# Performance work log

Hardware: AMD Instinct MI355X
Metric: run time of the kernel (lower is better)

Reference implementation:

```python
import jax, jax.numpy as jnp
import numpy as np

B, N, F, UNITS = 8, 2048, 64, 64

def setup_inputs() -> dict:
    key = jax.random.key(0)
    ks = jax.random.split(key, 7)
    inputs = jax.random.normal(ks[0], (B, N, F), dtype=jnp.float32)
    Dynamic_L = jax.random.normal(ks[1], (B, N, N), dtype=jnp.float32)
    W = jax.random.uniform(ks[2], (B, N, N, 3), dtype=jnp.float32)
    Geo = jax.random.normal(ks[3], (N, N), dtype=jnp.float32)
    KL = jax.random.normal(ks[4], (N, N), dtype=jnp.float32)
    # Dense(Units, tanh) params (glorot-ish scale)
    Wd = jax.random.normal(ks[5], (F, UNITS), dtype=jnp.float32) / np.sqrt(F)
    bd = jnp.zeros((UNITS,), dtype=jnp.float32)
    return {"inputs": inputs, "Dynamic_L": Dynamic_L, "W": W,
            "Geo": Geo, "KL": KL, "Wd": Wd, "bd": bd}

def reference(inputs, Dynamic_L, W, Geo, KL, Wd, bd):
    # Weighted fusion of three N x N matrices; Geo/KL broadcast over batch.
    Fusion = Dynamic_L * W[..., 0] + Geo[None] * W[..., 1] + KL[None] * W[..., 2]  # [B,N,N]
    Fusion = jax.nn.softmax(Fusion, axis=-1)
    G1 = jnp.einsum('bnm,bmf->bnf', Fusion, inputs)  # graph matmul [B,N,F]
    return jnp.tanh(G1 @ Wd + bd)  # Dense(Units, tanh) -> [B,N,UNITS]
```

## Files before the change

kernel.cpp:

```cpp
#include <hip/hip_runtime.h>
#include <hip/hip_fp16.h>

#define Nn 2048
#define Ff 64
#define Uu 64
#define NT 256
#define CW 256
#define NCH 8

typedef _Float16 f16x4 __attribute__((ext_vector_type(4)));
typedef _Float16 f16x8 __attribute__((ext_vector_type(8)));
typedef float    f32x4 __attribute__((ext_vector_type(4)));

#define MFMA32(a,b,c) __builtin_amdgcn_mfma_f32_16x16x32_f16(a,b,c,0,0,0)
#define G1S 68

__global__ __launch_bounds__(256) void transposeX(const float* __restrict__ X,
                                                  _Float16* __restrict__ Xt) {
    __shared__ _Float16 tile[64][65];
    const int b = blockIdx.x, kt = blockIdx.y;
    #pragma unroll
    for (int i = 0; i < 16; ++i) {
        int e  = i * 256 + threadIdx.x;
        int kk = e >> 6, ff = e & 63;
        tile[ff][kk] = (_Float16)X[((size_t)b * Nn + kt * 64 + kk) * Ff + ff];
    }
    __syncthreads();
    #pragma unroll
    for (int i = 0; i < 16; ++i) {
        int e  = i * 256 + threadIdx.x;
        int ff = e >> 6, kk = e & 63;
        Xt[((size_t)b * Ff + ff) * Nn + kt * 64 + kk] = tile[ff][kk];
    }
}

#define ISSUE_U(Vd,Vw0,Vw1,Vw2,Vg,Vk, C, U) {                 \
    const size_t _o = (size_t)(U) * Nn + (size_t)(C) * CW + (lane << 2); \
    Vd  = *(const float4*)(dP + _o);                          \
    Vw0 = *(const float4*)(wP + 3 * _o);                      \
    Vw1 = *(const float4*)(wP + 3 * _o + 4);                  \
    Vw2 = *(const float4*)(wP + 3 * _o + 8);                  \
    Vg  = *(const float4*)(gP + _o);                          \
    Vk  = *(const float4*)(kP + _o);                          \
}

#define CONSUME_U(Vd,Vw0,Vw1,Vw2,Vg,Vk, BUF, U) {                             \
    float _e0 = __expf(fminf(Vd.x*Vw0.x + Vg.x*Vw0.y + Vk.x*Vw0.z, 11.f));    \
    float _e1 = __expf(fminf(Vd.y*Vw0.w + Vg.y*Vw1.x + Vk.y*Vw1.y, 11.f));    \
    float _e2 = __expf(fminf(Vd.z*Vw1.z + Vg.z*Vw1.w + Vk.z*Vw2.x, 11.f));    \
    float _e3 = __expf(fminf(Vd.w*Vw2.y + Vg.w*Vw2.z + Vk.w*Vw2.w, 11.f));    \
    f16x4 _h = {(_Float16)_e0, (_Float16)_e1, (_Float16)_e2, (_Float16)_e3};  \
    rs[U] += (float)_h[0] + (float)_h[1] + (float)_h[2] + (float)_h[3];       \
    const int _ba = (p8 + (U)) * 512 + (lane << 3);                           \
    *(f16x4*)((char*)(BUF) + (_ba ^ (((U) & 7) << 4))) = _h;                  \
}

#define STAGE_BODY(BUF, C, PRE) {                          \
    CONSUME_U(Ad,Aw0,Aw1,Aw2,Ag,Ak, BUF, 0);               \
    ISSUE_U(Ad,Aw0,Aw1,Aw2,Ag,Ak, C, 2);                   \
    CONSUME_U(Bd,Bw0,Bw1,Bw2,Bg,Bk, BUF, 1);               \
    ISSUE_U(Bd,Bw0,Bw1,Bw2,Bg,Bk, C, 3);                   \
    CONSUME_U(Ad,Aw0,Aw1,Aw2,Ag,Ak, BUF, 2);               \
    ISSUE_U(Ad,Aw0,Aw1,Aw2,Ag,Ak, C, 4);                   \
    CONSUME_U(Bd,Bw0,Bw1,Bw2,Bg,Bk, BUF, 3);               \
    ISSUE_U(Bd,Bw0,Bw1,Bw2,Bg,Bk, C, 5);                   \
    CONSUME_U(Ad,Aw0,Aw1,Aw2,Ag,Ak, BUF, 4);               \
    ISSUE_U(Ad,Aw0,Aw1,Aw2,Ag,Ak, C, 6);                   \
    CONSUME_U(Bd,Bw0,Bw1,Bw2,Bg,Bk, BUF, 5);               \
    ISSUE_U(Bd,Bw0,Bw1,Bw2,Bg,Bk, C, 7);                   \
    CONSUME_U(Ad,Aw0,Aw1,Aw2,Ag,Ak, BUF, 6);               \
    if (PRE) { ISSUE_U(Ad,Aw0,Aw1,Aw2,Ag,Ak, (C)+1, 0); }  \
    CONSUME_U(Bd,Bw0,Bw1,Bw2,Bg,Bk, BUF, 7);               \
    if (PRE) { ISSUE_U(Bd,Bw0,Bw1,Bw2,Bg,Bk, (C)+1, 1); }  \
}

#define MFMA_CHUNK(BUF, C) {                                        \
    const char* _bc = (const char*)(BUF);                           \
    const _Float16* _x0 = xB0 + (size_t)(C) * CW;                   \
    const _Float16* _x1 = xB1 + (size_t)(C) * CW;                   \
    _Pragma("unroll")                                               \
    for (int kk = 0; kk < 8; ++kk) {                                \
        const int aa = r * 512 + kk * 64 + kg * 16;                 \
        f16x8 af = *(const f16x8*)(_bc + (aa ^ ((r & 7) << 4)));    \
        f16x8 b0 = *(const f16x8*)(_x0 + kk * 32);                  \
        f16x8 b1 = *(const f16x8*)(_x1 + kk * 32);                  \
        acc0 = MFMA32(af, b0, acc0);                                \
        acc1 = MFMA32(af, b1, acc1);                                \
    }                                                               \
}

__global__ __launch_bounds__(NT, 4) void fused_gcn(
    const _Float16* __restrict__ Xt,
    const float* __restrict__ Dyn,
    const float* __restrict__ Wf,
    const float* __restrict__ Geo,
    const float* __restrict__ KLm,
    const float* __restrict__ Wd,
    const float* __restrict__ bdv,
    float* __restrict__ out)
{
    __shared__ _Float16 Pb[2][16 * CW];
    __shared__ float wsumS[16];
    __shared__ float invS[16];
    __shared__ float g1[16 * G1S];

    const int t    = threadIdx.x;
    const int lane = t & 63;
    const int wid  = t >> 6;
    const int r    = lane & 15;
    const int kg   = lane >> 4;
    const int b    = blockIdx.x >> 7;
    const int n0   = (blockIdx.x & 127) << 4;

    const int p  = wid & 1;
    const int p8 = p << 3;
    const float* dP = Dyn + ((size_t)b * Nn + n0 + p8) * Nn;
    const float* wP = Wf  + ((size_t)b * Nn + n0 + p8) * (size_t)Nn * 3;
    const float* gP = Geo + (size_t)(n0 + p8) * Nn;
    const float* kP = KLm + (size_t)(n0 + p8) * Nn;

    const int cw = wid & 1;
    const _Float16* xB0 = Xt + (size_t)b * Ff * Nn
                        + (size_t)((cw * 2) * 16 + r) * Nn + (kg << 3);
    const _Float16* xB1 = xB0 + (size_t)16 * Nn;

    float rs[8] = {0.f,0.f,0.f,0.f,0.f,0.f,0.f,0.f};
    f32x4 acc0 = {0.f,0.f,0.f,0.f}, acc1 = {0.f,0.f,0.f,0.f};
    float4 Ad, Aw0, Aw1, Aw2, Ag, Ak;
    float4 Bd, Bw0, Bw1, Bw2, Bg, Bk;

    if (wid < 2) {
        ISSUE_U(Ad,Aw0,Aw1,Aw2,Ag,Ak, 0, 0);
        ISSUE_U(Bd,Bw0,Bw1,Bw2,Bg,Bk, 0, 1);
    }

    #pragma unroll 1
    for (int it = 0; it < NCH + 1; ++it) {
        if (wid < 2) {
            if (it < NCH) STAGE_BODY(&Pb[it & 1][0], it, (it + 1 < NCH));
        } else {
            if (it > 0) MFMA_CHUNK(&Pb[(it - 1) & 1][0], it - 1);
        }
        __syncthreads();
    }

    if (wid < 2) {
        #pragma unroll
        for (int u = 0; u < 8; ++u) {
            float v = rs[u];
            v += __shfl_xor(v, 1, 64);  v += __shfl_xor(v, 2, 64);
            v += __shfl_xor(v, 4, 64);  v += __shfl_xor(v, 8, 64);
            v += __shfl_xor(v, 16, 64); v += __shfl_xor(v, 32, 64);
            if (lane == 0) wsumS[p8 + u] = v;
        }
    }
    __syncthreads();
    if (t < 16) invS[t] = 1.0f / wsumS[t];
    __syncthreads();

    if (wid >= 2) {
        #pragma unroll
        for (int i = 0; i < 4; ++i) {
            const int ro = (kg << 2) + i;
            const float inv = invS[ro];
            g1[ro * G1S + (cw * 2) * 16 + r]       = acc0[i] * inv;
            g1[ro * G1S + (cw * 2 + 1) * 16 + r]   = acc1[i] * inv;
        }
    }
    __syncthreads();

    const int row0 = wid << 2;
    const float* g1r = g1 + row0 * G1S;
    float o0 = bdv[lane], o1 = o0, o2 = o0, o3 = o0;
    #pragma unroll 4
    for (int f = 0; f < Ff; ++f) {
        float wdv = Wd[f * Uu + lane];
        o0 += g1r[f]           * wdv;
        o1 += g1r[G1S + f]     * wdv;
        o2 += g1r[2 * G1S + f] * wdv;
        o3 += g1r[3 * G1S + f] * wdv;
    }
    float oo[4] = {o0, o1, o2, o3};
    #pragma unroll
    for (int i = 0; i < 4; ++i) {
        float x  = fminf(fmaxf(oo[i], -15.f), 15.f);
        float ex = __expf(2.f * x);
        out[((size_t)b * Nn + n0 + row0 + i) * Uu + lane] = (ex - 1.f) / (ex + 1.f);
    }
}

extern "C" void kernel_launch(void* const* d_in, const int* in_sizes, int n_in,
                              void* d_out, int out_size, void* d_ws, size_t ws_size,
                              hipStream_t stream) {
    const float* X   = (const float*)d_in[0];
    const float* Dyn = (const float*)d_in[1];
    const float* Wf  = (const float*)d_in[2];
    const float* Geo = (const float*)d_in[3];
    const float* KLm = (const float*)d_in[4];
    const float* Wd  = (const float*)d_in[5];
    const float* bdv = (const float*)d_in[6];
    float* out = (float*)d_out;

    _Float16* Xt = (_Float16*)d_ws;
    transposeX<<<dim3(8, Nn / 64), dim3(256), 0, stream>>>(X, Xt);
    fused_gcn<<<dim3(8 * (Nn / 16)), dim3(NT), 0, stream>>>(
        Xt, Dyn, Wf, Geo, KLm, Wd, bdv, out);
}
```

Measured before the change: 158.7 us.

## Stage inputs via global_load_lds double buffering with all waves computing

Replaces the producer/consumer wave split, where two waves computed exponentials and two ran MFMAs, with all four waves doing both. The Dyn/W/Geo/KL tiles are staged through direct global-to-LDS loads into double buffers. The chunk width shrinks to 64 columns over 32 iterations, and launch bounds drop to 2 blocks per SM to fit the larger LDS footprint. The aim is to hide HBM latency with asynchronous LDS loads and put all waves to work, at the cost of two barriers per much smaller chunk, more LDS use and possibly lower occupancy.

```diff
diff --git a/kernel.cpp b/kernel.cpp
--- a/kernel.cpp
+++ b/kernel.cpp
@@ -5,15 +5,19 @@
 #define Ff 64
 #define Uu 64
 #define NT 256
-#define CW 256
-#define NCH 8
+#define CW 64
+#define NCH 32
+#define G1S 68
 
 typedef _Float16 f16x4 __attribute__((ext_vector_type(4)));
 typedef _Float16 f16x8 __attribute__((ext_vector_type(8)));
 typedef float    f32x4 __attribute__((ext_vector_type(4)));
 
 #define MFMA32(a,b,c) __builtin_amdgcn_mfma_f32_16x16x32_f16(a,b,c,0,0,0)
-#define G1S 68
+
+#define GLD16(gp, lp) __builtin_amdgcn_global_load_lds(                      \
+    (const __attribute__((address_space(1))) void*)(gp),                     \
+    (__attribute__((address_space(3))) void*)(lp), 16, 0, 0)
 
 __global__ __launch_bounds__(256) void transposeX(const float* __restrict__ X,
                                                   _Float16* __restrict__ Xt) {
@@ -34,62 +38,22 @@
     }
 }
 
-#define ISSUE_U(Vd,Vw0,Vw1,Vw2,Vg,Vk, C, U) {                 \
-    const size_t _o = (size_t)(U) * Nn + (size_t)(C) * CW + (lane << 2); \
-    Vd  = *(const float4*)(dP + _o);                          \
-    Vw0 = *(const float4*)(wP + 3 * _o);                      \
-    Vw1 = *(const float4*)(wP + 3 * _o + 4);                  \
-    Vw2 = *(const float4*)(wP + 3 * _o + 8);                  \
-    Vg  = *(const float4*)(gP + _o);                          \
-    Vk  = *(const float4*)(kP + _o);                          \
-}
-
-#define CONSUME_U(Vd,Vw0,Vw1,Vw2,Vg,Vk, BUF, U) {                             \
-    float _e0 = __expf(fminf(Vd.x*Vw0.x + Vg.x*Vw0.y + Vk.x*Vw0.z, 11.f));    \
-    float _e1 = __expf(fminf(Vd.y*Vw0.w + Vg.y*Vw1.x + Vk.y*Vw1.y, 11.f));    \
-    float _e2 = __expf(fminf(Vd.z*Vw1.z + Vg.z*Vw1.w + Vk.z*Vw2.x, 11.f));    \
-    float _e3 = __expf(fminf(Vd.w*Vw2.y + Vg.w*Vw2.z + Vk.w*Vw2.w, 11.f));    \
-    f16x4 _h = {(_Float16)_e0, (_Float16)_e1, (_Float16)_e2, (_Float16)_e3};  \
-    rs[U] += (float)_h[0] + (float)_h[1] + (float)_h[2] + (float)_h[3];       \
-    const int _ba = (p8 + (U)) * 512 + (lane << 3);                           \
-    *(f16x4*)((char*)(BUF) + (_ba ^ (((U) & 7) << 4))) = _h;                  \
-}
-
-#define STAGE_BODY(BUF, C, PRE) {                          \
-    CONSUME_U(Ad,Aw0,Aw1,Aw2,Ag,Ak, BUF, 0);               \
-    ISSUE_U(Ad,Aw0,Aw1,Aw2,Ag,Ak, C, 2);                   \
-    CONSUME_U(Bd,Bw0,Bw1,Bw2,Bg,Bk, BUF, 1);               \
-    ISSUE_U(Bd,Bw0,Bw1,Bw2,Bg,Bk, C, 3);                   \
-    CONSUME_U(Ad,Aw0,Aw1,Aw2,Ag,Ak, BUF, 2);               \
-    ISSUE_U(Ad,Aw0,Aw1,Aw2,Ag,Ak, C, 4);                   \
-    CONSUME_U(Bd,Bw0,Bw1,Bw2,Bg,Bk, BUF, 3);               \
-    ISSUE_U(Bd,Bw0,Bw1,Bw2,Bg,Bk, C, 5);                   \
-    CONSUME_U(Ad,Aw0,Aw1,Aw2,Ag,Ak, BUF, 4);               \
-    ISSUE_U(Ad,Aw0,Aw1,Aw2,Ag,Ak, C, 6);                   \
-    CONSUME_U(Bd,Bw0,Bw1,Bw2,Bg,Bk, BUF, 5);               \
-    ISSUE_U(Bd,Bw0,Bw1,Bw2,Bg,Bk, C, 7);                   \
-    CONSUME_U(Ad,Aw0,Aw1,Aw2,Ag,Ak, BUF, 6);               \
-    if (PRE) { ISSUE_U(Ad,Aw0,Aw1,Aw2,Ag,Ak, (C)+1, 0); }  \
-    CONSUME_U(Bd,Bw0,Bw1,Bw2,Bg,Bk, BUF, 7);               \
-    if (PRE) { ISSUE_U(Bd,Bw0,Bw1,Bw2,Bg,Bk, (C)+1, 1); }  \
-}
-
-#define MFMA_CHUNK(BUF, C) {                                        \
-    const char* _bc = (const char*)(BUF);                           \
-    const _Float16* _x0 = xB0 + (size_t)(C) * CW;                   \
-    const _Float16* _x1 = xB1 + (size_t)(C) * CW;                   \
-    _Pragma("unroll")                                               \
-    for (int kk = 0; kk < 8; ++kk) {                                \
-        const int aa = r * 512 + kk * 64 + kg * 16;                 \
-        f16x8 af = *(const f16x8*)(_bc + (aa ^ ((r & 7) << 4)));    \
-        f16x8 b0 = *(const f16x8*)(_x0 + kk * 32);                  \
-        f16x8 b1 = *(const f16x8*)(_x1 + kk * 32);                  \
-        acc0 = MFMA32(af, b0, acc0);                                \
-        acc1 = MFMA32(af, b1, acc1);                                \
-    }                                                               \
-}
-
-__global__ __launch_bounds__(NT, 4) void fused_gcn(
+#define STAGE_ISSUE(P) {                                       \
+    char* _db = (char*)&Db[P][0] + wid * 1024;                 \
+    char* _gb = (char*)&Gb[P][0] + wid * 1024;                 \
+    char* _kb = (char*)&Kb[P][0] + wid * 1024;                 \
+    char* _wb = (char*)&Wb[P][0] + wid * 3072;                 \
+    GLD16(dG, _db);                                            \
+    GLD16(gG, _gb);                                            \
+    GLD16(kG, _kb);                                            \
+    GLD16(wG0, _wb);                                           \
+    GLD16(wG1, _wb + 1024);                                    \
+    GLD16(wG2, _wb + 2048);                                    \
+    dG += 256; gG += 256; kG += 256;                           \
+    wG0 += 768; wG1 += 768; wG2 += 768;                        \
+}
+
+__global__ __launch_bounds__(NT, 2) void fused_gcn(
     const _Float16* __restrict__ Xt,
     const float* __restrict__ Dyn,
     const float* __restrict__ Wf,
@@ -99,10 +63,14 @@
     const float* __restrict__ bdv,
     float* __restrict__ out)
 {
-    __shared__ _Float16 Pb[2][16 * CW];
-    __shared__ float wsumS[16];
-    __shared__ float invS[16];
-    __shared__ float g1[16 * G1S];
+    __shared__ float   Db[2][16 * 64];
+    __shared__ float   Wb[2][16 * 192];
+    __shared__ float   Gb[2][16 * 64];
+    __shared__ float   Kb[2][16 * 64];
+    __shared__ _Float16 Pb[2][16 * 64];
+    __shared__ float   g1[16 * G1S];
+    __shared__ float   wsumS[16];
+    __shared__ float   invS[16];
 
     const int t    = threadIdx.x;
     const int lane = t & 63;
@@ -112,60 +80,98 @@
     const int b    = blockIdx.x >> 7;
     const int n0   = (blockIdx.x & 127) << 4;
 
-    const int p  = wid & 1;
-    const int p8 = p << 3;
-    const float* dP = Dyn + ((size_t)b * Nn + n0 + p8) * Nn;
-    const float* wP = Wf  + ((size_t)b * Nn + n0 + p8) * (size_t)Nn * 3;
-    const float* gP = Geo + (size_t)(n0 + p8) * Nn;
-    const float* kP = KLm + (size_t)(n0 + p8) * Nn;
-
-    const int cw = wid & 1;
-    const _Float16* xB0 = Xt + (size_t)b * Ff * Nn
-                        + (size_t)((cw * 2) * 16 + r) * Nn + (kg << 3);
-    const _Float16* xB1 = xB0 + (size_t)16 * Nn;
-
-    float rs[8] = {0.f,0.f,0.f,0.f,0.f,0.f,0.f,0.f};
-    f32x4 acc0 = {0.f,0.f,0.f,0.f}, acc1 = {0.f,0.f,0.f,0.f};
-    float4 Ad, Aw0, Aw1, Aw2, Ag, Ak;
-    float4 Bd, Bw0, Bw1, Bw2, Bg, Bk;
-
-    if (wid < 2) {
-        ISSUE_U(Ad,Aw0,Aw1,Aw2,Ag,Ak, 0, 0);
-        ISSUE_U(Bd,Bw0,Bw1,Bw2,Bg,Bk, 0, 1);
-    }
+    const int lrow = lane >> 4, lq = lane & 15;
+    const char* dG = (const char*)(Dyn + ((size_t)b * Nn + n0 + 4 * wid) * Nn)
+                     + (size_t)lrow * (Nn * 4) + lq * 16;
+    const char* gG = (const char*)(Geo + (size_t)(n0 + 4 * wid) * Nn)
+                     + (size_t)lrow * (Nn * 4) + lq * 16;
+    const char* kG = (const char*)(KLm + (size_t)(n0 + 4 * wid) * Nn)
+                     + (size_t)lrow * (Nn * 4) + lq * 16;
+    const char* wbase = (const char*)(Wf + ((size_t)b * Nn + n0 + 4 * wid) * (size_t)Nn * 3);
+    const int lin0 = lane * 16;
+    const int lin1 = 1024 + lane * 16;
+    const int lin2 = 2048 + lane * 16;
+    const int rw0 = (lin0 >= 768) ? 1 : 0;
+    const int rw1 = (lin1 >= 1536) ? 2 : 1;
+    const int rw2 = (lin2 >= 2304) ? 3 : 2;
+    const char* wG0 = wbase + (size_t)rw0 * (Nn * 12) + (lin0 - rw0 * 768);
+    const char* wG1 = wbase + (size_t)rw1 * (Nn * 12) + (lin1 - rw1 * 768);
+    const char* wG2 = wbase + (size_t)rw2 * (Nn * 12) + (lin2 - rw2 * 768);
+
+    const _Float16* xw = Xt + (size_t)b * Ff * Nn
+                       + (size_t)(wid * 16 + r) * Nn + (kg << 3);
+
+    const int erow = t >> 4, eq = t & 15;
+
+    f32x4 acc = {0.f, 0.f, 0.f, 0.f};
+    float rs = 0.f;
+
+    STAGE_ISSUE(0);
+    asm volatile("s_waitcnt vmcnt(0)" ::: "memory");
+    __builtin_amdgcn_s_barrier();
 
     #pragma unroll 1
-    for (int it = 0; it < NCH + 1; ++it) {
-        if (wid < 2) {
-            if (it < NCH) STAGE_BODY(&Pb[it & 1][0], it, (it + 1 < NCH));
-        } else {
-            if (it > 0) MFMA_CHUNK(&Pb[(it - 1) & 1][0], it - 1);
+    for (int c = 0; c < NCH; ++c) {
+        const int pc = c & 1;
+
+        f16x8 bf0 = *(const f16x8*)(xw);
+        f16x8 bf1 = *(const f16x8*)(xw + 32);
+        xw += 64;
+        __builtin_amdgcn_sched_barrier(0);
+
+        if (c + 1 < NCH) STAGE_ISSUE(pc ^ 1);
+        __builtin_amdgcn_sched_barrier(0);
+
+        {
+            const float* dd = &Db[pc][erow * 64 + eq * 4];
+            const float* gg = &Gb[pc][erow * 64 + eq * 4];
+            const float* kk = &Kb[pc][erow * 64 + eq * 4];
+            const float* ww = &Wb[pc][erow * 192 + eq * 12];
+            float4 dv = *(const float4*)dd;
+            float4 gv = *(const float4*)gg;
+            float4 kv = *(const float4*)kk;
+            float4 w0 = *(const float4*)ww;
+            float4 w1 = *(const float4*)(ww + 4);
+            float4 w2 = *(const float4*)(ww + 8);
+            float e0 = __expf(fminf(dv.x*w0.x + gv.x*w0.y + kv.x*w0.z, 11.f));
+            float e1 = __expf(fminf(dv.y*w0.w + gv.y*w1.x + kv.y*w1.y, 11.f));
+            float e2 = __expf(fminf(dv.z*w1.z + gv.z*w1.w + kv.z*w2.x, 11.f));
+            float e3 = __expf(fminf(dv.w*w2.y + gv.w*w2.z + kv.w*w2.w, 11.f));
+            f16x4 h = {(_Float16)e0, (_Float16)e1, (_Float16)e2, (_Float16)e3};
+            rs += (float)h[0] + (float)h[1] + (float)h[2] + (float)h[3];
+            *(f16x4*)((char*)&Pb[pc][0]
+                      + ((erow * 128 + eq * 8) ^ ((erow & 7) << 4))) = h;
         }
-        __syncthreads();
-    }
-
-    if (wid < 2) {
-        #pragma unroll
-        for (int u = 0; u < 8; ++u) {
-            float v = rs[u];
-            v += __shfl_xor(v, 1, 64);  v += __shfl_xor(v, 2, 64);
-            v += __shfl_xor(v, 4, 64);  v += __shfl_xor(v, 8, 64);
-            v += __shfl_xor(v, 16, 64); v += __shfl_xor(v, 32, 64);
-            if (lane == 0) wsumS[p8 + u] = v;
+
+        asm volatile("s_waitcnt lgkmcnt(0)" ::: "memory");
+        __builtin_amdgcn_sched_barrier(0);
+        __builtin_amdgcn_s_barrier();
+
+        {
+            const char* pbuf = (const char*)&Pb[pc][0];
+            f16x8 af0 = *(const f16x8*)(pbuf + ((r * 128 + kg * 16) ^ ((r & 7) << 4)));
+            f16x8 af1 = *(const f16x8*)(pbuf + ((r * 128 + 64 + kg * 16) ^ ((r & 7) << 4)));
+            acc = MFMA32(af0, bf0, acc);
+            acc = MFMA32(af1, bf1, acc);
         }
-    }
+
+        asm volatile("s_waitcnt vmcnt(0)" ::: "memory");
+        __builtin_amdgcn_sched_barrier(0);
+        __builtin_amdgcn_s_barrier();
+    }
+
+    float v = rs;
+    v += __shfl_xor(v, 1, 64); v += __shfl_xor(v, 2, 64);
+    v += __shfl_xor(v, 4, 64); v += __shfl_xor(v, 8, 64);
+    if ((lane & 15) == 0) wsumS[(wid << 2) + (lane >> 4)] = v;
     __syncthreads();
     if (t < 16) invS[t] = 1.0f / wsumS[t];
     __syncthreads();
 
-    if (wid >= 2) {
-        #pragma unroll
-        for (int i = 0; i < 4; ++i) {
-            const int ro = (kg << 2) + i;
-            const float inv = invS[ro];
-            g1[ro * G1S + (cw * 2) * 16 + r]       = acc0[i] * inv;
-            g1[ro * G1S + (cw * 2 + 1) * 16 + r]   = acc1[i] * inv;
-        }
+    #pragma unroll
+    for (int i = 0; i < 4; ++i) {
+        const int ro = (kg << 2) + i;
+        g1[ro * G1S + (wid << 4) + r] = acc[i] * invS[ro];
     }
     __syncthreads();
 
```

Measured after the change: 127.3 us (median of 2 runs). -19.8%, faster.
